# Optimization experiments

Hardware: AMD Instinct MI355X
Metric: run time of the kernel (lower is better)

The kernel has to match this reference:

```python
import jax, jax.numpy as jnp
import numpy as np

B, S, N, NODE_IN, IN_DIM, H, EMB = 2048, 168, 64, 16, 16, 64, 4
# N == H is required by the original broadcast `attention_score * station_features_emb`


def setup_inputs() -> dict:
    key = jax.random.key(0)
    ks = jax.random.split(key, 24)
    p = lambda i, shape, s=0.05: jax.random.normal(ks[i], shape, jnp.float32) * s
    inp = {
        "local_node": jax.random.normal(ks[0], (B, NODE_IN), jnp.float32),
        "station_nodes": jax.random.normal(ks[1], (B, N, NODE_IN), jnp.float32),
        "station_features": jax.random.normal(ks[2], (B, S, IN_DIM), jnp.float32),
    }
    weather = jax.random.randint(ks[3], (B, S, 1), 0, 12)
    wind = jax.random.randint(ks[4], (B, S, 1), 0, 10)
    month = jax.random.randint(ks[5], (B, S, 1), 1, 13)  # 1-indexed in source
    day = jax.random.randint(ks[6], (B, S, 1), 1, 8)
    hour = jax.random.randint(ks[7], (B, S, 1), 1, 25)
    inp["station_emb"] = jnp.stack([weather, wind, month, day, hour], axis=-1).astype(jnp.int32)  # (B,S,1,5)
    inp.update(
        emb_weather=p(8, (12, EMB), 1.0), emb_wind=p(9, (10, EMB), 1.0),
        emb_month=p(10, (12, EMB), 1.0), emb_day=p(11, (7, EMB), 1.0),
        emb_hour=p(12, (24, EMB), 1.0),
        W_nodes=p(13, (H, NODE_IN)), b_nodes=jnp.zeros((H,), jnp.float32),
        W_attn=p(14, (1, 2 * H)), b_attn=jnp.zeros((1,), jnp.float32),
        W_d1=p(15, (H // 2, IN_DIM + 5 * EMB)), b_d1=jnp.zeros((H // 2,), jnp.float32),
        W_d2=p(16, (H, H // 2)), b_d2=jnp.zeros((H,), jnp.float32),
        Wih0=p(17, (3 * H, 2 * H)), Whh0=p(18, (3 * H, H)),
        bih0=jnp.zeros((3 * H,), jnp.float32), bhh0=jnp.zeros((3 * H,), jnp.float32),
        Wih1=p(19, (3 * H, H)), Whh1=p(20, (3 * H, H)),
        bih1=jnp.zeros((3 * H,), jnp.float32), bhh1=jnp.zeros((3 * H,), jnp.float32),
        W_pred=p(21, (1, 2 * H)), b_pred=jnp.zeros((1,), jnp.float32),
    )
    return inp


def _gru_layer(x, Wih, Whh, bih, bhh):
    # x: (B,S,Din); PyTorch GRU gate math, gates ordered (r,z,n).
    xg = jnp.einsum('bsd,gd->sbg', x, Wih) + bih  # (S,B,3H) precomputed input gates
    h0 = jnp.zeros((x.shape[0], Whh.shape[1]), x.dtype)

    def step(h, xg_t):
        gh = h @ Whh.T + bhh
        xr, xz, xn = jnp.split(xg_t, 3, axis=-1)
        hr, hz, hn = jnp.split(gh, 3, axis=-1)
        r = jax.nn.sigmoid(xr + hr)
        z = jax.nn.sigmoid(xz + hz)
        n = jnp.tanh(xn + r * hn)
        h_new = (1.0 - z) * n + z * h
        return h_new, h_new

    h_last, hs = jax.lax.scan(step, h0, xg)
    return jnp.swapaxes(hs, 0, 1), h_last  # (B,S,H), (B,H)


def _forward(local_node, station_nodes, station_features, station_emb,
             emb_weather, emb_wind, emb_month, emb_day, emb_hour,
             W_nodes, b_nodes, W_attn, b_attn, W_d1, b_d1, W_d2, b_d2,
             Wih0, Whh0, bih0, bhh0, Wih1, Whh1, bih1, bhh1, W_pred, b_pred):
    local_emb = jnp.tanh(local_node @ W_nodes.T + b_nodes)          # (B,H)
    site_emb = jnp.tanh(station_nodes @ W_nodes.T + b_nodes)        # (B,N,H)
    # attn(cat(local, site)) == local@Wl + site@Ws + b, vectorized over sites
    Wl, Ws = W_attn[0, :H], W_attn[0, H:]
    energies = site_emb @ Ws + (local_emb @ Wl)[:, None] + b_attn[0]  # (B,N)
    attn = jax.nn.softmax(energies, axis=-1)                          # (B,N), N==H

    e = lambda tab, idx: tab[idx].reshape(idx.shape[0], idx.shape[1], -1)  # (B,S,EMB)
    cat = jnp.concatenate([
        station_features,
        e(emb_weather, station_emb[..., 0]),
        e(emb_wind, station_emb[..., 1]),
        e(emb_month, station_emb[..., 2] - 1),
        e(emb_day, station_emb[..., 3] - 1),
        e(emb_hour, station_emb[..., 4] - 1),
    ], axis=-1)                                                      # (B,S,IN_DIM+20)
    h1 = jnp.tanh(cat @ W_d1.T + b_d1)
    sfe = jnp.tanh(h1 @ W_d2.T + b_d2)                               # (B,S,H)

    local_feature = attn[:, None, :] * sfe                           # broadcast over seq
    features = jnp.concatenate([local_feature, sfe], axis=-1)        # (B,S,2H)

    out0, hf0 = _gru_layer(features, Wih0, Whh0, bih0, bhh0)
    out1, hf1 = _gru_layer(out0, Wih1, Whh1, bih1, bhh1)
    hidden = jnp.concatenate([hf0, hf1], axis=-1)                    # (B,2H)
    pred = jnp.tanh(hidden @ W_pred.T + b_pred)                      # (B,1)
    return pred


def reference(local_node, station_nodes, station_features, station_emb,
              emb_weather, emb_wind, emb_month, emb_day, emb_hour,
              W_nodes, b_nodes, W_attn, b_attn, W_d1, b_d1, W_d2, b_d2,
              Wih0, Whh0, bih0, bhh0, Wih1, Whh1, bih1, bhh1, W_pred, b_pred):
    return _forward(local_node, station_nodes, station_features, station_emb,
                    emb_weather, emb_wind, emb_month, emb_day, emb_hour,
                    W_nodes, b_nodes, W_attn, b_attn, W_d1, b_d1, W_d2, b_d2,
                    Wih0, Whh0, bih0, bhh0, Wih1, Whh1, bih1, bhh1, W_pred, b_pred)
```

## Files before the change

### kernel.cpp

```cpp
#include <hip/hip_runtime.h>
#include <cstdint>
#include <cstddef>

#define B_ 2048
#define S_ 168
#define NT_ 5376

typedef _Float16 h2_t __attribute__((ext_vector_type(2)));
typedef _Float16 f16x8 __attribute__((ext_vector_type(8)));
typedef float f32x4 __attribute__((ext_vector_type(4)));
typedef unsigned int u32;

__device__ __forceinline__ unsigned pack_h2f(float a, float b){
    h2_t v; v.x = (_Float16)a; v.y = (_Float16)b;
    return __builtin_bit_cast(unsigned, v);
}
__device__ __forceinline__ float fast_exp(float x){
    return __builtin_amdgcn_exp2f(x * 1.44269504088896340736f);
}
__device__ __forceinline__ float fast_sigmoid(float x){
    return __builtin_amdgcn_rcpf(1.0f + fast_exp(-x));
}
__device__ __forceinline__ float fast_tanh(float x){
    return 1.0f - 2.0f * __builtin_amdgcn_rcpf(1.0f + fast_exp(2.0f * x));
}
__device__ __forceinline__ void wsync(){
    asm volatile("s_waitcnt lgkmcnt(0)" ::: "memory");
    __builtin_amdgcn_wave_barrier();
}
__device__ __forceinline__ void bar_lds(){
    asm volatile("s_waitcnt lgkmcnt(0)\n\ts_barrier" ::: "memory");
}
__device__ __forceinline__ f32x4 mfma16(uint4 a, uint4 b, f32x4 c){
    return __builtin_amdgcn_mfma_f32_16x16x32_f16(
        __builtin_bit_cast(f16x8, a), __builtin_bit_cast(f16x8, b), c, 0, 0, 0);
}
__device__ __forceinline__ uint4 load_bfrag(const float* __restrict__ W, int ldk,
                                            int o, int kk0, int kmax){
    float w[8];
    #pragma unroll
    for (int e = 0; e < 8; ++e){
        int kk = kk0 + e;
        w[e] = (kk < kmax) ? W[o*ldk + kk] : 0.f;
    }
    uint4 r;
    r.x = pack_h2f(w[0], w[1]); r.y = pack_h2f(w[2], w[3]);
    r.z = pack_h2f(w[4], w[5]); r.w = pack_h2f(w[6], w[7]);
    return r;
}

__global__ void nbst_attn(const float* __restrict__ sn, const float* __restrict__ Wn,
                          const float* __restrict__ bn, const float* __restrict__ Wa,
                          float* __restrict__ attnO){
    __shared__ float WnL[64*16];
    __shared__ float WsL[64];
    __shared__ float bnL[64];
    const int tid = threadIdx.x;
    for (int e = tid; e < 1024; e += 256) WnL[e] = Wn[e];
    if (tid < 64){ WsL[tid] = Wa[64 + tid]; bnL[tid] = bn[tid]; }
    __syncthreads();
    const int wv = tid >> 6, l = tid & 63;
    const int b = blockIdx.x * 4 + wv;
    const float* xp = sn + ((size_t)b * 64 + l) * 16;
    float x[16];
    #pragma unroll
    for (int k = 0; k < 16; ++k) x[k] = xp[k];
    float e_i = 0.f;
    for (int h = 0; h < 64; ++h){
        float acc = bnL[h];
        #pragma unroll
        for (int k = 0; k < 16; ++k) acc += x[k] * WnL[h*16 + k];
        e_i += fast_tanh(acc) * WsL[h];
    }
    float m = e_i;
    #pragma unroll
    for (int s = 32; s >= 1; s >>= 1) m = fmaxf(m, __shfl_xor(m, s));
    float p = fast_exp(e_i - m);
    float ssum = p;
    #pragma unroll
    for (int s = 32; s >= 1; s >>= 1) ssum += __shfl_xor(ssum, s);
    attnO[(size_t)b*64 + l] = p * __builtin_amdgcn_rcpf(ssum);
}

#define A0_CAT 0
#define A0_H1  2304
#define A0_FT  3584
#define A0_WM  7936
#define A0_EMB 9984
#define A0_ATT 10244
#define A0_TOT 11268

__global__ __launch_bounds__(256, 2)
void nbst_mlpxg0(const float* __restrict__ sf, const int* __restrict__ se,
                 const float* __restrict__ e0, const float* __restrict__ e1,
                 const float* __restrict__ e2, const float* __restrict__ e3,
                 const float* __restrict__ e4,
                 const float* __restrict__ Wd1, const float* __restrict__ bd1,
                 const float* __restrict__ Wd2, const float* __restrict__ bd2,
                 const float* __restrict__ Wih0, const float* __restrict__ attnI,
                 u32* __restrict__ xg0F)
{
    __shared__ u32 sm[A0_TOT];
    float* smF = reinterpret_cast<float*>(sm);
    const int tid = threadIdx.x;
    const int w = tid >> 6, l = tid & 63;
    const int q = l >> 4, c = l & 15;

    for (int e = tid; e < 260; e += 256){
        float v;
        if (e < 48)       v = e0[e];
        else if (e < 88)  v = e1[e-48];
        else if (e < 136) v = e2[e-88];
        else if (e < 164) v = e3[e-136];
        else              v = e4[e-164];
        smF[A0_EMB + e] = v;
    }
    for (int f = w; f < 8; f += 4){
        uint4 fr;
        if (f < 4){ int n = f >> 1, ks = f & 1;
                    fr = load_bfrag(Wd1, 36, 16*n + c, 32*ks + 8*q, 36); }
        else      { int n = f - 4;
                    fr = load_bfrag(Wd2, 32, 16*n + c, 8*q, 32); }
        *reinterpret_cast<uint4*>(sm + A0_WM + (f*64 + l)*4) = fr;
    }
    uint4 bw[3][4];
    #pragma unroll
    for (int nn = 0; nn < 3; ++nn)
        #pragma unroll
        for (int ks = 0; ks < 4; ++ks)
            bw[nn][ks] = load_bfrag(Wih0, 128, 16*(w + 4*nn) + c, 32*ks + 8*q, 128);
    for (int e = tid; e < 64*18; e += 256){
        int row = e / 18, j = 18 + e % 18;
        sm[A0_CAT + row*36 + j] = 0u;
    }
    const float bb10 = bd1[c],  bb11 = bd1[16+c];
    const float bb20 = bd2[c],  bb21 = bd2[16+c];
    const float bb22 = bd2[32+c], bb23 = bd2[48+c];
    __syncthreads();

    for (int tile = blockIdx.x; tile < NT_; tile += gridDim.x){
        const int gb = tile / 42, tb = tile % 42;
        for (int e = tid; e < 1024; e += 256)
            smF[A0_ATT + e] = attnI[(size_t)(16*gb)*64 + e];
        for (int e = tid; e < 64*18; e += 256){
            int row = e / 18, j = e % 18;
            int R = (16*gb + (row & 15))*S_ + 4*tb + (row >> 4);
            float c0, c1;
            if (j < 8){
                c0 = sf[(size_t)R*16 + 2*j]; c1 = sf[(size_t)R*16 + 2*j + 1];
            } else {
                int jj = j - 8, ebl = jj >> 1, d0 = (jj & 1) * 2;
                int idx = se[(size_t)R*5 + ebl] - (ebl >= 2 ? 1 : 0);
                const int toff = (ebl==0)?0:(ebl==1)?48:(ebl==2)?88:(ebl==3)?136:164;
                c0 = smF[A0_EMB + toff + idx*4 + d0];
                c1 = smF[A0_EMB + toff + idx*4 + d0 + 1];
            }
            sm[A0_CAT + row*36 + j] = pack_h2f(c0, c1);
        }
        __syncthreads();

        {
            f32x4 c1a[2];
            c1a[0] = (f32x4){bb10, bb10, bb10, bb10};
            c1a[1] = (f32x4){bb11, bb11, bb11, bb11};
            #pragma unroll
            for (int ks = 0; ks < 2; ++ks){
                uint4 a = *reinterpret_cast<const uint4*>(
                    sm + A0_CAT + (16*w + c)*36 + ks*16 + 4*q);
                #pragma unroll
                for (int n = 0; n < 2; ++n)
                    c1a[n] = mfma16(a, *reinterpret_cast<const uint4*>(
                        sm + A0_WM + ((n*2 + ks)*64 + l)*4), c1a[n]);
            }
            #pragma unroll
            for (int n = 0; n < 2; ++n)
                #pragma unroll
                for (int j = 0; j < 4; ++j){
                    float v = fast_tanh(c1a[n][j]);
                    float vp = __shfl_xor(v, 1);
                    if (!(l & 1))
                        sm[A0_H1 + (16*w + 4*q + j)*20 + 8*n + (c >> 1)] = pack_h2f(v, vp);
                }
        }
        wsync();

        {
            uint4 a = *reinterpret_cast<const uint4*>(
                sm + A0_H1 + (16*w + c)*20 + 4*q);
            f32x4 c2[4];
            c2[0] = (f32x4){bb20, bb20, bb20, bb20};
            c2[1] = (f32x4){bb21, bb21, bb21, bb21};
            c2[2] = (f32x4){bb22, bb22, bb22, bb22};
            c2[3] = (f32x4){bb23, bb23, bb23, bb23};
            #pragma unroll
            for (int n = 0; n < 4; ++n)
                c2[n] = mfma16(a, *reinterpret_cast<const uint4*>(
                    sm + A0_WM + ((4 + n)*64 + l)*4), c2[n]);
            #pragma unroll
            for (int n = 0; n < 4; ++n)
                #pragma unroll
                for (int j = 0; j < 4; ++j){
                    float s  = fast_tanh(c2[n][j]);
                    float fa = smF[A0_ATT + (4*q + j)*64 + 16*n + c] * s;
                    float sp  = __shfl_xor(s, 1);
                    float fap = __shfl_xor(fa, 1);
                    if (!(l & 1)){
                        int row = 16*w + 4*q + j;
                        int ci = 8*n + (c >> 1);
                        sm[A0_FT + row*68 + ci]      = pack_h2f(fa, fap);
                        sm[A0_FT + row*68 + 32 + ci] = pack_h2f(s, sp);
                    }
                }
        }
        __syncthreads();

        #pragma unroll
        for (int m = 0; m < 4; ++m){
            uint4 af[4];
            #pragma unroll
            for (int ks = 0; ks < 4; ++ks)
                af[ks] = *reinterpret_cast<const uint4*>(
                    sm + A0_FT + (16*m + c)*68 + ks*16 + 4*q);
            f32x4 acc[3];
            #pragma unroll
            for (int nn = 0; nn < 3; ++nn) acc[nn] = (f32x4){0.f, 0.f, 0.f, 0.f};
            #pragma unroll
            for (int ks = 0; ks < 4; ++ks)
                #pragma unroll
                for (int nn = 0; nn < 3; ++nn)
                    acc[nn] = mfma16(af[ks], bw[nn][ks], acc[nn]);
            size_t base = ((size_t)(gb*S_ + 4*tb + m))*1536 + (size_t)w*384 + (size_t)l*6;
            uint2 s01, s23, s45;
            s01.x = pack_h2f(acc[0][0], acc[0][1]); s01.y = pack_h2f(acc[0][2], acc[0][3]);
            s23.x = pack_h2f(acc[1][0], acc[1][1]); s23.y = pack_h2f(acc[1][2], acc[1][3]);
            s45.x = pack_h2f(acc[2][0], acc[2][1]); s45.y = pack_h2f(acc[2][2], acc[2][3]);
            *reinterpret_cast<uint2*>(xg0F + base + 0) = s01;
            *reinterpret_cast<uint2*>(xg0F + base + 2) = s23;
            *reinterpret_cast<uint2*>(xg0F + base + 4) = s45;
        }
        __syncthreads();
    }
}

#define RW0 6912
#define RW1 13056
#define RHB (RW0 + RW1)
#define RF_TOT (RHB + 2048)

__global__ __launch_bounds__(256, 1)
void nbst_recf(const u32* __restrict__ xg0F,
               const float* __restrict__ Whh0,
               const float* __restrict__ bih0, const float* __restrict__ bhh0,
               const float* __restrict__ Wih1, const float* __restrict__ Whh1,
               const float* __restrict__ bih1, const float* __restrict__ bhh1,
               const float* __restrict__ Wpred, const float* __restrict__ bpred,
               float* __restrict__ outp)
{
    extern __shared__ u32 sm[];
    u32* smw0 = sm;
    u32* smw1 = sm + RW0;
    u32* HB   = sm + RHB;
    const int tid = threadIdx.x, w = tid >> 6, l = tid & 63;
    const int q = l >> 4, c = l & 15;
    const int g = blockIdx.x, B0 = g*16;

    for (int e = tid; e < 192*32; e += 256){
        int row = e >> 5, k = e & 31;
        smw0[row*36 + k] = pack_h2f(Whh0[row*64 + 2*k], Whh0[row*64 + 2*k + 1]);
    }
    for (int e = tid; e < 192*64; e += 256){
        int row = e / 64, kp = e % 64;
        smw1[row*68 + kp] = (kp < 32)
            ? pack_h2f(Wih1[row*64 + 2*kp],      Wih1[row*64 + 2*kp + 1])
            : pack_h2f(Whh1[row*64 + 2*(kp-32)], Whh1[row*64 + 2*(kp-32) + 1]);
    }
    for (int e = tid; e < 2048; e += 256) HB[e] = 0u;
    __syncthreads();

    const int gr = 16*w + c, gz = 64 + 16*w + c, gn = 128 + 16*w + c;
    uint4 aBR[2], aBZ[2], aBHN[2];
    #pragma unroll
    for (int ks = 0; ks < 2; ++ks){
        aBR[ks]  = *reinterpret_cast<const uint4*>(smw0 + gr*36 + 16*ks + 4*q);
        aBZ[ks]  = *reinterpret_cast<const uint4*>(smw0 + gz*36 + 16*ks + 4*q);
        aBHN[ks] = *reinterpret_cast<const uint4*>(smw0 + gn*36 + 16*ks + 4*q);
    }
    uint4 xBR[2], xBZ[2], xBXN[2], hBR[2], hBZ[2], hBHN[2];
    #pragma unroll
    for (int ks = 0; ks < 2; ++ks){
        xBR[ks] = *reinterpret_cast<const uint4*>(smw1 + gr*68 + 16*ks + 4*q);
        xBZ[ks] = *reinterpret_cast<const uint4*>(smw1 + gz*68 + 16*ks + 4*q);
        hBR[ks] = *reinterpret_cast<const uint4*>(smw1 + gr*68 + 32 + 16*ks + 4*q);
        hBZ[ks] = *reinterpret_cast<const uint4*>(smw1 + gz*68 + 32 + 16*ks + 4*q);
    }
    xBXN[0] = *reinterpret_cast<const uint4*>(smw1 + gn*68 +      4*q);
    xBXN[1] = *reinterpret_cast<const uint4*>(smw1 + gn*68 + 16 + 4*q);
    hBHN[0] = *reinterpret_cast<const uint4*>(smw1 + gn*68 + 32 + 4*q);
    hBHN[1] = *reinterpret_cast<const uint4*>(smw1 + gn*68 + 48 + 4*q);

    const float br0 = bih0[gr] + bhh0[gr], bz0 = bih0[gz] + bhh0[gz];
    const float bxn0 = bih0[gn], bhn0 = bhh0[gn];
    const float br1 = bih1[gr] + bhh1[gr], bz1 = bih1[gz] + bhh1[gz];
    const float bxn1 = bih1[gn], bhn1 = bhh1[gn];

    const int rd0 = (c*32 + 4*q)      ^ ((c & 7) << 2);
    const int rd1 = (c*32 + 4*q + 16) ^ ((c & 7) << 2);
    int wri[4];
    #pragma unroll
    for (int j = 0; j < 4; ++j){
        int row = 4*q + j;
        wri[j] = (row*64 + 16*w + c) ^ ((row & 7) << 3);
    }

    const u32* xb = xg0F + (size_t)g * S_ * 1536 + (size_t)w * 384 + (size_t)l * 6;
    uint2 x0a, x0b, x0c, x1a, x1b, x1c, x2a, x2b, x2c, x3a, x3b, x3c;
    {
        const u32* p0 = xb;
        const u32* p1 = xb + 1536;
        const u32* p2 = xb + 2*1536;
        const u32* p3 = xb + 3*1536;
        x0a = *(const uint2*)(p0+0); x0b = *(const uint2*)(p0+2); x0c = *(const uint2*)(p0+4);
        x1a = *(const uint2*)(p1+0); x1b = *(const uint2*)(p1+2); x1c = *(const uint2*)(p1+4);
        x2a = *(const uint2*)(p2+0); x2b = *(const uint2*)(p2+2); x2c = *(const uint2*)(p2+4);
        x3a = *(const uint2*)(p3+0); x3b = *(const uint2*)(p3+2); x3c = *(const uint2*)(p3+4);
    }
    float h0r0 = 0.f, h0r1 = 0.f, h0r2 = 0.f, h0r3 = 0.f;
    float h1r0 = 0.f, h1r1 = 0.f, h1r2 = 0.f, h1r3 = 0.f;
    __syncthreads();

#define RSTEP(I, XA, XB, XC, DOL1) do{                                          \
    const int i_ = (I);                                                         \
    const u32* hp0_ = HB + ((i_ + 1) & 1) * 512;                                \
    const u32* hp1_ = HB + 1024 + ((i_ + 1) & 1) * 512;                         \
    uint4 hA0a_ = *(const uint4*)(hp0_ + rd0);                                  \
    uint4 hA0b_ = *(const uint4*)(hp0_ + rd1);                                  \
    uint4 hA1a_ = *(const uint4*)(hp1_ + rd0);                                  \
    uint4 hA1b_ = *(const uint4*)(hp1_ + rd1);                                  \
    {                                                       \
        f32x4 aRh_ = {0,0,0,0}, aZh_ = {0,0,0,0}, aHN_ = {0,0,0,0};             \
        aRh_ = mfma16(hA0a_, aBR[0], aRh_);  aRh_ = mfma16(hA0b_, aBR[1], aRh_);\
        aZh_ = mfma16(hA0a_, aBZ[0], aZh_);  aZh_ = mfma16(hA0b_, aBZ[1], aZh_);\
        aHN_ = mfma16(hA0a_, aBHN[0], aHN_); aHN_ = mfma16(hA0b_, aBHN[1], aHN_);\
        h2_t xR01_ = __builtin_bit_cast(h2_t, (XA).x);                          \
        h2_t xR23_ = __builtin_bit_cast(h2_t, (XA).y);                          \
        h2_t xZ01_ = __builtin_bit_cast(h2_t, (XB).x);                          \
        h2_t xZ23_ = __builtin_bit_cast(h2_t, (XB).y);                          \
        h2_t xN01_ = __builtin_bit_cast(h2_t, (XC).x);                          \
        h2_t xN23_ = __builtin_bit_cast(h2_t, (XC).y);                          \
        _Float16* hw_ = (_Float16*)(HB + (i_ & 1) * 512);                       \
        float rg_, zg_, ng_;                                                    \
        rg_ = fast_sigmoid((float)xR01_.x + aRh_[0] + br0);                     \
        zg_ = fast_sigmoid((float)xZ01_.x + aZh_[0] + bz0);                     \
        ng_ = fast_tanh((float)xN01_.x + bxn0 + rg_*(aHN_[0] + bhn0));          \
        h0r0 = (1.f - zg_)*ng_ + zg_*h0r0; hw_[wri[0]] = (_Float16)h0r0;        \
        rg_ = fast_sigmoid((float)xR01_.y + aRh_[1] + br0);                     \
        zg_ = fast_sigmoid((float)xZ01_.y + aZh_[1] + bz0);                     \
        ng_ = fast_tanh((float)xN01_.y + bxn0 + rg_*(aHN_[1] + bhn0));          \
        h0r1 = (1.f - zg_)*ng_ + zg_*h0r1; hw_[wri[1]] = (_Float16)h0r1;        \
        rg_ = fast_sigmoid((float)xR23_.x + aRh_[2] + br0);                     \
        zg_ = fast_sigmoid((float)xZ23_.x + aZh_[2] + bz0);                     \
        ng_ = fast_tanh((float)xN23_.x + bxn0 + rg_*(aHN_[2] + bhn0));          \
        h0r2 = (1.f - zg_)*ng_ + zg_*h0r2; hw_[wri[2]] = (_Float16)h0r2;        \
        rg_ = fast_sigmoid((float)xR23_.y + aRh_[3] + br0);                     \
        zg_ = fast_sigmoid((float)xZ23_.y + aZh_[3] + bz0);                     \
        ng_ = fast_tanh((float)xN23_.y + bxn0 + rg_*(aHN_[3] + bhn0));          \
        h0r3 = (1.f - zg_)*ng_ + zg_*h0r3; hw_[wri[3]] = (_Float16)h0r3;        \
    }                                                                           \
    if (DOL1){                         \
        f32x4 cR_ = {0,0,0,0}, cZ_ = {0,0,0,0}, cXN_ = {0,0,0,0}, cHN_ = {0,0,0,0};\
        cR_  = mfma16(hA0a_, xBR[0], cR_);   cR_  = mfma16(hA0b_, xBR[1], cR_); \
        cZ_  = mfma16(hA0a_, xBZ[0], cZ_);   cZ_  = mfma16(hA0b_, xBZ[1], cZ_); \
        cXN_ = mfma16(hA0a_, xBXN[0], cXN_); cXN_ = mfma16(hA0b_, xBXN[1], cXN_);\
        cR_  = mfma16(hA1a_, hBR[0], cR_);   cR_  = mfma16(hA1b_, hBR[1], cR_); \
        cZ_  = mfma16(hA1a_, hBZ[0], cZ_);   cZ_  = mfma16(hA1b_, hBZ[1], cZ_); \
        cHN_ = mfma16(hA1a_, hBHN[0], cHN_); cHN_ = mfma16(hA1b_, hBHN[1], cHN_);\
        _Float16* hw_ = (_Float16*)(HB + 1024 + (i_ & 1) * 512);                \
        float rg_, zg_, ng_;                                                    \
        rg_ = fast_sigmoid(cR_[0] + br1); zg_ = fast_sigmoid(cZ_[0] + bz1);     \
        ng_ = fast_tanh(cXN_[0] + bxn1 + rg_*(cHN_[0] + bhn1));                 \
        h1r0 = (1.f - zg_)*ng_ + zg_*h1r0; hw_[wri[0]] = (_Float16)h1r0;        \
        rg_ = fast_sigmoid(cR_[1] + br1); zg_ = fast_sigmoid(cZ_[1] + bz1);     \
        ng_ = fast_tanh(cXN_[1] + bxn1 + rg_*(cHN_[1] + bhn1));                 \
        h1r1 = (1.f - zg_)*ng_ + zg_*h1r1; hw_[wri[1]] = (_Float16)h1r1;        \
        rg_ = fast_sigmoid(cR_[2] + br1); zg_ = fast_sigmoid(cZ_[2] + bz1);     \
        ng_ = fast_tanh(cXN_[2] + bxn1 + rg_*(cHN_[2] + bhn1));                 \
        h1r2 = (1.f - zg_)*ng_ + zg_*h1r2; hw_[wri[2]] = (_Float16)h1r2;        \
        rg_ = fast_sigmoid(cR_[3] + br1); zg_ = fast_sigmoid(cZ_[3] + bz1);     \
        ng_ = fast_tanh(cXN_[3] + bxn1 + rg_*(cHN_[3] + bhn1));                 \
        h1r3 = (1.f - zg_)*ng_ + zg_*h1r3; hw_[wri[3]] = (_Float16)h1r3;        \
    }                                                                           \
    {          \
        int tn_ = (i_ + 4 < S_) ? i_ + 4 : S_ - 1;                              \
        const u32* xp_ = xb + (size_t)tn_ * 1536;                               \
        (XA) = *(const uint2*)(xp_ + 0);                                        \
        (XB) = *(const uint2*)(xp_ + 2);                                        \
        (XC) = *(const uint2*)(xp_ + 4);                                        \
    }                                                                           \
    bar_lds();                                                                  \
} while(0)

    RSTEP(0, x0a, x0b, x0c, 0);
    RSTEP(1, x1a, x1b, x1c, 1);
    RSTEP(2, x2a, x2b, x2c, 1);
    RSTEP(3, x3a, x3b, x3c, 1);
    #pragma unroll 1
    for (int i4 = 1; i4 < 42; ++i4){
        const int ib = 4*i4;
        RSTEP(ib + 0, x0a, x0b, x0c, 1);
        RSTEP(ib + 1, x1a, x1b, x1c, 1);
        RSTEP(ib + 2, x2a, x2b, x2c, 1);
        RSTEP(ib + 3, x3a, x3b, x3c, 1);
    }
    {
        const u32* hp0_ = HB + 512;
        const u32* hp1_ = HB + 1024 + 512;
        uint4 hA0a_ = *(const uint4*)(hp0_ + rd0);
        uint4 hA0b_ = *(const uint4*)(hp0_ + rd1);
        uint4 hA1a_ = *(const uint4*)(hp1_ + rd0);
        uint4 hA1b_ = *(const uint4*)(hp1_ + rd1);
        f32x4 cR_ = {0,0,0,0}, cZ_ = {0,0,0,0}, cXN_ = {0,0,0,0}, cHN_ = {0,0,0,0};
        cR_  = mfma16(hA0a_, xBR[0], cR_);   cR_  = mfma16(hA0b_, xBR[1], cR_);
        cZ_  = mfma16(hA0a_, xBZ[0], cZ_);   cZ_  = mfma16(hA0b_, xBZ[1], cZ_);
        cXN_ = mfma16(hA0a_, xBXN[0], cXN_); cXN_ = mfma16(hA0b_, xBXN[1], cXN_);
        cR_  = mfma16(hA1a_, hBR[0], cR_);   cR_  = mfma16(hA1b_, hBR[1], cR_);
        cZ_  = mfma16(hA1a_, hBZ[0], cZ_);   cZ_  = mfma16(hA1b_, hBZ[1], cZ_);
        cHN_ = mfma16(hA1a_, hBHN[0], cHN_); cHN_ = mfma16(hA1b_, hBHN[1], cHN_);
        float rg_, zg_, ng_;
        rg_ = fast_sigmoid(cR_[0] + br1); zg_ = fast_sigmoid(cZ_[0] + bz1);
        ng_ = fast_tanh(cXN_[0] + bxn1 + rg_*(cHN_[0] + bhn1));
        h1r0 = (1.f - zg_)*ng_ + zg_*h1r0;
        rg_ = fast_sigmoid(cR_[1] + br1); zg_ = fast_sigmoid(cZ_[1] + bz1);
        ng_ = fast_tanh(cXN_[1] + bxn1 + rg_*(cHN_[1] + bhn1));
        h1r1 = (1.f - zg_)*ng_ + zg_*h1r1;
        rg_ = fast_sigmoid(cR_[2] + br1); zg_ = fast_sigmoid(cZ_[2] + bz1);
        ng_ = fast_tanh(cXN_[2] + bxn1 + rg_*(cHN_[2] + bhn1));
        h1r2 = (1.f - zg_)*ng_ + zg_*h1r2;
        rg_ = fast_sigmoid(cR_[3] + br1); zg_ = fast_sigmoid(cZ_[3] + bz1);
        ng_ = fast_tanh(cXN_[3] + bxn1 + rg_*(cHN_[3] + bhn1));
        h1r3 = (1.f - zg_)*ng_ + zg_*h1r3;
    }

    __syncthreads();
    float* s0 = reinterpret_cast<float*>(sm);
    float* s1 = reinterpret_cast<float*>(sm) + 1024;
    #pragma unroll
    for (int j = 0; j < 4; ++j){
        int row = 4*q + j;
        float h0v = (j == 0) ? h0r0 : (j == 1) ? h0r1 : (j == 2) ? h0r2 : h0r3;
        float h1v = (j == 0) ? h1r0 : (j == 1) ? h1r1 : (j == 2) ? h1r2 : h1r3;
        s0[row*64 + 16*w + c] = h0v;
        s1[row*64 + 16*w + c] = h1v;
    }
    __syncthreads();
    {
        const int r = tid >> 4, cg = tid & 15;
        const float* hp0 = s0 + r*64 + 4*cg;
        const float* hp1 = s1 + r*64 + 4*cg;
        const float* wp0 = Wpred + 4*cg;
        const float* wp1 = Wpred + 64 + 4*cg;
        float part = hp0[0]*wp0[0] + hp0[1]*wp0[1] + hp0[2]*wp0[2] + hp0[3]*wp0[3]
                   + hp1[0]*wp1[0] + hp1[1]*wp1[1] + hp1[2]*wp1[2] + hp1[3]*wp1[3];
        part += __shfl_xor(part, 8);
        part += __shfl_xor(part, 4);
        part += __shfl_xor(part, 2);
        part += __shfl_xor(part, 1);
        if (cg == 0) outp[B0 + r] = fast_tanh(part + bpred[0]);
    }
#undef RSTEP
}

extern "C" void kernel_launch(void* const* d_in, const int* in_sizes, int n_in,
                              void* d_out, int out_size, void* d_ws, size_t ws_size,
                              hipStream_t stream) {
    (void)in_sizes; (void)n_in; (void)out_size; (void)ws_size;
    const float* station_nodes    = (const float*)d_in[1];
    const float* station_features = (const float*)d_in[2];
    const int*   station_emb      = (const int*)d_in[3];
    const float* e0 = (const float*)d_in[4];
    const float* e1 = (const float*)d_in[5];
    const float* e2 = (const float*)d_in[6];
    const float* e3 = (const float*)d_in[7];
    const float* e4 = (const float*)d_in[8];
    const float* W_nodes = (const float*)d_in[9];
    const float* b_nodes = (const float*)d_in[10];
    const float* W_attn  = (const float*)d_in[11];
    const float* W_d1 = (const float*)d_in[13];
    const float* b_d1 = (const float*)d_in[14];
    const float* W_d2 = (const float*)d_in[15];
    const float* b_d2 = (const float*)d_in[16];
    const float* Wih0 = (const float*)d_in[17];
    const float* Whh0 = (const float*)d_in[18];
    const float* bih0 = (const float*)d_in[19];
    const float* bhh0 = (const float*)d_in[20];
    const float* Wih1 = (const float*)d_in[21];
    const float* Whh1 = (const float*)d_in[22];
    const float* bih1 = (const float*)d_in[23];
    const float* bhh1 = (const float*)d_in[24];
    const float* W_pred = (const float*)d_in[25];
    const float* b_pred = (const float*)d_in[26];
    float* outp = (float*)d_out;

    char* ws = (char*)d_ws;
    float* attnW = (float*)ws;
    u32*   xg0F  = (u32*)(ws + (1u<<20));

    hipFuncSetAttribute((const void*)nbst_recf,
                        hipFuncAttributeMaxDynamicSharedMemorySize, 96*1024);

    nbst_attn<<<dim3(512), dim3(256), 0, stream>>>(station_nodes, W_nodes, b_nodes, W_attn, attnW);
    nbst_mlpxg0<<<dim3(768), dim3(256), 0, stream>>>(
        station_features, station_emb, e0, e1, e2, e3, e4,
        W_d1, b_d1, W_d2, b_d2, Wih0, attnW, xg0F);
    nbst_recf<<<dim3(128), dim3(256), RF_TOT*4, stream>>>(
        xg0F, Whh0, bih0, bhh0, Wih1, Whh1, bih1, bhh1,
        W_pred, b_pred, outp);
}
```

Baseline: 226.2 us.

## Pack two batch groups per recurrent block and fold gate biases into MFMA accumulators

The recurrent GRU kernel now launches 64 blocks of 512 threads instead of 128 blocks of 256. Each block runs two independent 16-row batch groups, which share one LDS copy of the weights and keep separate hidden-state buffers. This lets two latency-bound recurrence chains interleave on the same SIMDs and halves the weight staging. The cost is block-wide barriers across 8 waves and only 64 CUs in use. Gate biases are also loaded as the initial MFMA accumulator values, which removes per-element bias adds in the gate math.

```diff
diff --git a/kernel.cpp b/kernel.cpp
--- a/kernel.cpp
+++ b/kernel.cpp
@@ -245,9 +245,9 @@
 #define RW0 6912
 #define RW1 13056
 #define RHB (RW0 + RW1)
-#define RF_TOT (RHB + 2048)
-
-__global__ __launch_bounds__(256, 1)
+#define RF_TOT (RHB + 4096)
+
+__global__ __launch_bounds__(512, 1)
 void nbst_recf(const u32* __restrict__ xg0F,
                const float* __restrict__ Whh0,
                const float* __restrict__ bih0, const float* __restrict__ bhh0,
@@ -259,22 +259,24 @@
     extern __shared__ u32 sm[];
     u32* smw0 = sm;
     u32* smw1 = sm + RW0;
-    u32* HB   = sm + RHB;
-    const int tid = threadIdx.x, w = tid >> 6, l = tid & 63;
+    const int tid = threadIdx.x;
+    const int w8 = tid >> 6, l = tid & 63;
+    const int grp = w8 >> 2, w = w8 & 3;
     const int q = l >> 4, c = l & 15;
-    const int g = blockIdx.x, B0 = g*16;
-
-    for (int e = tid; e < 192*32; e += 256){
+    const int g = blockIdx.x * 2 + grp;
+    u32* HB = sm + RHB + grp * 2048;
+
+    for (int e = tid; e < 192*32; e += 512){
         int row = e >> 5, k = e & 31;
         smw0[row*36 + k] = pack_h2f(Whh0[row*64 + 2*k], Whh0[row*64 + 2*k + 1]);
     }
-    for (int e = tid; e < 192*64; e += 256){
+    for (int e = tid; e < 192*64; e += 512){
         int row = e / 64, kp = e % 64;
         smw1[row*68 + kp] = (kp < 32)
             ? pack_h2f(Wih1[row*64 + 2*kp],      Wih1[row*64 + 2*kp + 1])
             : pack_h2f(Whh1[row*64 + 2*(kp-32)], Whh1[row*64 + 2*(kp-32) + 1]);
     }
-    for (int e = tid; e < 2048; e += 256) HB[e] = 0u;
+    for (int e = tid; e < 4096; e += 512) sm[RHB + e] = 0u;
     __syncthreads();
 
     const int gr = 16*w + c, gz = 64 + 16*w + c, gn = 128 + 16*w + c;
@@ -336,8 +338,10 @@
     uint4 hA0b_ = *(const uint4*)(hp0_ + rd1);                                  \
     uint4 hA1a_ = *(const uint4*)(hp1_ + rd0);                                  \
     uint4 hA1b_ = *(const uint4*)(hp1_ + rd1);                                  \
-    {                                                       \
-        f32x4 aRh_ = {0,0,0,0}, aZh_ = {0,0,0,0}, aHN_ = {0,0,0,0};             \
+    {                  \
+        f32x4 aRh_ = {br0,br0,br0,br0};                                         \
+        f32x4 aZh_ = {bz0,bz0,bz0,bz0};                                         \
+        f32x4 aHN_ = {bhn0,bhn0,bhn0,bhn0};                                     \
         aRh_ = mfma16(hA0a_, aBR[0], aRh_);  aRh_ = mfma16(hA0b_, aBR[1], aRh_);\
         aZh_ = mfma16(hA0a_, aBZ[0], aZh_);  aZh_ = mfma16(hA0b_, aBZ[1], aZh_);\
         aHN_ = mfma16(hA0a_, aBHN[0], aHN_); aHN_ = mfma16(hA0b_, aBHN[1], aHN_);\
@@ -349,25 +353,28 @@
         h2_t xN23_ = __builtin_bit_cast(h2_t, (XC).y);                          \
         _Float16* hw_ = (_Float16*)(HB + (i_ & 1) * 512);                       \
         float rg_, zg_, ng_;                                                    \
-        rg_ = fast_sigmoid((float)xR01_.x + aRh_[0] + br0);                     \
-        zg_ = fast_sigmoid((float)xZ01_.x + aZh_[0] + bz0);                     \
-        ng_ = fast_tanh((float)xN01_.x + bxn0 + rg_*(aHN_[0] + bhn0));          \
+        rg_ = fast_sigmoid((float)xR01_.x + aRh_[0]);                           \
+        zg_ = fast_sigmoid((float)xZ01_.x + aZh_[0]);                           \
+        ng_ = fast_tanh((float)xN01_.x + bxn0 + rg_*aHN_[0]);                   \
         h0r0 = (1.f - zg_)*ng_ + zg_*h0r0; hw_[wri[0]] = (_Float16)h0r0;        \
-        rg_ = fast_sigmoid((float)xR01_.y + aRh_[1] + br0);                     \
-        zg_ = fast_sigmoid((float)xZ01_.y + aZh_[1] + bz0);                     \
-        ng_ = fast_tanh((float)xN01_.y + bxn0 + rg_*(aHN_[1] + bhn0));          \
+        rg_ = fast_sigmoid((float)xR01_.y + aRh_[1]);                           \
+        zg_ = fast_sigmoid((float)xZ01_.y + aZh_[1]);                           \
+        ng_ = fast_tanh((float)xN01_.y + bxn0 + rg_*aHN_[1]);                   \
         h0r1 = (1.f - zg_)*ng_ + zg_*h0r1; hw_[wri[1]] = (_Float16)h0r1;        \
-        rg_ = fast_sigmoid((float)xR23_.x + aRh_[2] + br0);                     \
-        zg_ = fast_sigmoid((float)xZ23_.x + aZh_[2] + bz0);                     \
-        ng_ = fast_tanh((float)xN23_.x + bxn0 + rg_*(aHN_[2] + bhn0));          \
+        rg_ = fast_sigmoid((float)xR23_.x + aRh_[2]);                           \
+        zg_ = fast_sigmoid((float)xZ23_.x + aZh_[2]);                           \
+        ng_ = fast_tanh((float)xN23_.x + bxn0 + rg_*aHN_[2]);                   \
         h0r2 = (1.f - zg_)*ng_ + zg_*h0r2; hw_[wri[2]] = (_Float16)h0r2;        \
-        rg_ = fast_sigmoid((float)xR23_.y + aRh_[3] + br0);                     \
-        zg_ = fast_sigmoid((float)xZ23_.y + aZh_[3] + bz0);                     \
-        ng_ = fast_tanh((float)xN23_.y + bxn0 + rg_*(aHN_[3] + bhn0));          \
+        rg_ = fast_sigmoid((float)xR23_.y + aRh_[3]);                           \
+        zg_ = fast_sigmoid((float)xZ23_.y + aZh_[3]);                           \
+        ng_ = fast_tanh((float)xN23_.y + bxn0 + rg_*aHN_[3]);                   \
         h0r3 = (1.f - zg_)*ng_ + zg_*h0r3; hw_[wri[3]] = (_Float16)h0r3;        \
     }                                                                           \
     if (DOL1){                         \
-        f32x4 cR_ = {0,0,0,0}, cZ_ = {0,0,0,0}, cXN_ = {0,0,0,0}, cHN_ = {0,0,0,0};\
+        f32x4 cR_  = {br1,br1,br1,br1};                                         \
+        f32x4 cZ_  = {bz1,bz1,bz1,bz1};                                         \
+        f32x4 cXN_ = {bxn1,bxn1,bxn1,bxn1};                                     \
+        f32x4 cHN_ = {bhn1,bhn1,bhn1,bhn1};                                     \
         cR_  = mfma16(hA0a_, xBR[0], cR_);   cR_  = mfma16(hA0b_, xBR[1], cR_); \
         cZ_  = mfma16(hA0a_, xBZ[0], cZ_);   cZ_  = mfma16(hA0b_, xBZ[1], cZ_); \
         cXN_ = mfma16(hA0a_, xBXN[0], cXN_); cXN_ = mfma16(hA0b_, xBXN[1], cXN_);\
@@ -376,17 +383,17 @@
         cHN_ = mfma16(hA1a_, hBHN[0], cHN_); cHN_ = mfma16(hA1b_, hBHN[1], cHN_);\
         _Float16* hw_ = (_Float16*)(HB + 1024 + (i_ & 1) * 512);                \
         float rg_, zg_, ng_;                                                    \
-        rg_ = fast_sigmoid(cR_[0] + br1); zg_ = fast_sigmoid(cZ_[0] + bz1);     \
-        ng_ = fast_tanh(cXN_[0] + bxn1 + rg_*(cHN_[0] + bhn1));                 \
+        rg_ = fast_sigmoid(cR_[0]); zg_ = fast_sigmoid(cZ_[0]);                 \
+        ng_ = fast_tanh(cXN_[0] + rg_*cHN_[0]);                                 \
         h1r0 = (1.f - zg_)*ng_ + zg_*h1r0; hw_[wri[0]] = (_Float16)h1r0;        \
-        rg_ = fast_sigmoid(cR_[1] + br1); zg_ = fast_sigmoid(cZ_[1] + bz1);     \
-        ng_ = fast_tanh(cXN_[1] + bxn1 + rg_*(cHN_[1] + bhn1));                 \
+        rg_ = fast_sigmoid(cR_[1]); zg_ = fast_sigmoid(cZ_[1]);                 \
+        ng_ = fast_tanh(cXN_[1] + rg_*cHN_[1]);                                 \
         h1r1 = (1.f - zg_)*ng_ + zg_*h1r1; hw_[wri[1]] = (_Float16)h1r1;        \
-        rg_ = fast_sigmoid(cR_[2] + br1); zg_ = fast_sigmoid(cZ_[2] + bz1);     \
-        ng_ = fast_tanh(cXN_[2] + bxn1 + rg_*(cHN_[2] + bhn1));                 \
+        rg_ = fast_sigmoid(cR_[2]); zg_ = fast_sigmoid(cZ_[2]);                 \
+        ng_ = fast_tanh(cXN_[2] + rg_*cHN_[2]);                                 \
         h1r2 = (1.f - zg_)*ng_ + zg_*h1r2; hw_[wri[2]] = (_Float16)h1r2;        \
-        rg_ = fast_sigmoid(cR_[3] + br1); zg_ = fast_sigmoid(cZ_[3] + bz1);     \
-        ng_ = fast_tanh(cXN_[3] + bxn1 + rg_*(cHN_[3] + bhn1));                 \
+        rg_ = fast_sigmoid(cR_[3]); zg_ = fast_sigmoid(cZ_[3]);                 \
+        ng_ = fast_tanh(cXN_[3] + rg_*cHN_[3]);                                 \
         h1r3 = (1.f - zg_)*ng_ + zg_*h1r3; hw_[wri[3]] = (_Float16)h1r3;        \
     }                                                                           \
     {          \
@@ -418,7 +425,10 @@
         uint4 hA0b_ = *(const uint4*)(hp0_ + rd1);
         uint4 hA1a_ = *(const uint4*)(hp1_ + rd0);
         uint4 hA1b_ = *(const uint4*)(hp1_ + rd1);
-        f32x4 cR_ = {0,0,0,0}, cZ_ = {0,0,0,0}, cXN_ = {0,0,0,0}, cHN_ = {0,0,0,0};
+        f32x4 cR_  = {br1,br1,br1,br1};
+        f32x4 cZ_  = {bz1,bz1,bz1,bz1};
+        f32x4 cXN_ = {bxn1,bxn1,bxn1,bxn1};
+        f32x4 cHN_ = {bhn1,bhn1,bhn1,bhn1};
         cR_  = mfma16(hA0a_, xBR[0], cR_);   cR_  = mfma16(hA0b_, xBR[1], cR_);
         cZ_  = mfma16(hA0a_, xBZ[0], cZ_);   cZ_  = mfma16(hA0b_, xBZ[1], cZ_);
         cXN_ = mfma16(hA0a_, xBXN[0], cXN_); cXN_ = mfma16(hA0b_, xBXN[1], cXN_);
@@ -426,26 +436,26 @@
         cZ_  = mfma16(hA1a_, hBZ[0], cZ_);   cZ_  = mfma16(hA1b_, hBZ[1], cZ_);
         cHN_ = mfma16(hA1a_, hBHN[0], cHN_); cHN_ = mfma16(hA1b_, hBHN[1], cHN_);
         float rg_, zg_, ng_;
-        rg_ = fast_sigmoid(cR_[0] + br1); zg_ = fast_sigmoid(cZ_[0] + bz1);
-        ng_ = fast_tanh(cXN_[0] + bxn1 + rg_*(cHN_[0] + bhn1));
+        rg_ = fast_sigmoid(cR_[0]); zg_ = fast_sigmoid(cZ_[0]);
+        ng_ = fast_tanh(cXN_[0] + rg_*cHN_[0]);
         h1r0 = (1.f - zg_)*ng_ + zg_*h1r0;
-        rg_ = fast_sigmoid(cR_[1] + br1); zg_ = fast_sigmoid(cZ_[1] + bz1);
-        ng_ = fast_tanh(cXN_[1] + bxn1 + rg_*(cHN_[1] + bhn1));
+        rg_ = fast_sigmoid(cR_[1]); zg_ = fast_sigmoid(cZ_[1]);
+        ng_ = fast_tanh(cXN_[1] + rg_*cHN_[1]);
         h1r1 = (1.f - zg_)*ng_ + zg_*h1r1;
-        rg_ = fast_sigmoid(cR_[2] + br1); zg_ = fast_sigmoid(cZ_[2] + bz1);
-        ng_ = fast_tanh(cXN_[2] + bxn1 + rg_*(cHN_[2] + bhn1));
+        rg_ = fast_sigmoid(cR_[2]); zg_ = fast_sigmoid(cZ_[2]);
+        ng_ = fast_tanh(cXN_[2] + rg_*cHN_[2]);
         h1r2 = (1.f - zg_)*ng_ + zg_*h1r2;
-        rg_ = fast_sigmoid(cR_[3] + br1); zg_ = fast_sigmoid(cZ_[3] + bz1);
-        ng_ = fast_tanh(cXN_[3] + bxn1 + rg_*(cHN_[3] + bhn1));
+        rg_ = fast_sigmoid(cR_[3]); zg_ = fast_sigmoid(cZ_[3]);
+        ng_ = fast_tanh(cXN_[3] + rg_*cHN_[3]);
         h1r3 = (1.f - zg_)*ng_ + zg_*h1r3;
     }
 
     __syncthreads();
     float* s0 = reinterpret_cast<float*>(sm);
-    float* s1 = reinterpret_cast<float*>(sm) + 1024;
+    float* s1 = reinterpret_cast<float*>(sm) + 2048;
     #pragma unroll
     for (int j = 0; j < 4; ++j){
-        int row = 4*q + j;
+        int row = grp*16 + 4*q + j;
         float h0v = (j == 0) ? h0r0 : (j == 1) ? h0r1 : (j == 2) ? h0r2 : h0r3;
         float h1v = (j == 0) ? h1r0 : (j == 1) ? h1r1 : (j == 2) ? h1r2 : h1r3;
         s0[row*64 + 16*w + c] = h0v;
@@ -464,7 +474,7 @@
         part += __shfl_xor(part, 4);
         part += __shfl_xor(part, 2);
         part += __shfl_xor(part, 1);
-        if (cg == 0) outp[B0 + r] = fast_tanh(part + bpred[0]);
+        if (cg == 0) outp[blockIdx.x*32 + r] = fast_tanh(part + bpred[0]);
     }
 #undef RSTEP
 }
@@ -505,13 +515,13 @@
     u32*   xg0F  = (u32*)(ws + (1u<<20));
 
     hipFuncSetAttribute((const void*)nbst_recf,
-                        hipFuncAttributeMaxDynamicSharedMemorySize, 96*1024);
+                        hipFuncAttributeMaxDynamicSharedMemorySize, 112*1024);
 
     nbst_attn<<<dim3(512), dim3(256), 0, stream>>>(station_nodes, W_nodes, b_nodes, W_attn, attnW);
     nbst_mlpxg0<<<dim3(768), dim3(256), 0, stream>>>(
         station_features, station_emb, e0, e1, e2, e3, e4,
         W_d1, b_d1, W_d2, b_d2, Wih0, attnW, xg0F);
-    nbst_recf<<<dim3(128), dim3(256), RF_TOT*4, stream>>>(
+    nbst_recf<<<dim3(64), dim3(512), RF_TOT*4, stream>>>(
         xg0F, Whh0, bih0, bhh0, Wih1, Whh1, bih1, bhh1,
         W_pred, b_pred, outp);
 }
```

New measurement: 264.1 us. 16.8% more time.
